# Performance work log

Measured on AMD Instinct MI355X. Metric: run time of the kernel, lower is better.

## Reference

```python
import jax, jax.numpy as jnp
from jax import lax
import numpy as np

# Config matching init_kwargs
NUM_CLASSES = 19
K = 200               # keep_k_centers
NMS_KERNEL = 9
CENTER_THR = 0.1
LABEL_DIV = 256
VOID = 255
STUFF_AREA = 4096
THING_IDS = np.array([11, 12, 13, 14, 15, 16, 17, 18])
IS_THING = jnp.zeros(NUM_CLASSES, bool).at[jnp.asarray(THING_IDS)].set(True)


def _process_one(logits, heat, offset):
    # logits [C,H,W], heat [1,H,W], offset [2,H,W]
    C, H, W = logits.shape
    sem = jnp.argmax(logits, axis=0).astype(jnp.int32)          # [H,W]
    h = heat[0]
    ht = jnp.where(h > CENTER_THR, h, 0.0)
    pad = NMS_KERNEL // 2
    # torch max_pool2d pads implicitly with -inf
    pooled = lax.reduce_window(ht, -jnp.inf, lax.max,
                               (NMS_KERNEL, NMS_KERNEL), (1, 1),
                               ((pad, pad), (pad, pad)))
    nms = jnp.where(ht == pooled, ht, 0.0)                      # [H,W]
    flat = nms.reshape(-1)
    scores, idx = lax.top_k(flat, K)                            # fixed-size center set
    valid = scores > 0.0
    num_pos = jnp.sum(flat > 0.0)
    # Match torch ordering: if more than K peaks -> topk (descending-score) order;
    # otherwise nonzero() row-major order. Invalid slots pushed to the end.
    big = jnp.int32(H * W + K)
    order_key = jnp.where(valid,
                          jnp.where(num_pos > K,
                                    jnp.arange(K, dtype=jnp.int32),
                                    idx.astype(jnp.int32)),
                          big)
    perm = jnp.argsort(order_key)
    idx = idx[perm]
    valid = valid[perm]
    FAR = 1e9  # invalid centers placed infinitely far away
    cy = jnp.where(valid, (idx // W).astype(jnp.float32), FAR)
    cx = jnp.where(valid, (idx % W).astype(jnp.float32), FAR)
    ty = jnp.arange(H, dtype=jnp.float32)[:, None] + offset[0]  # [H,W]
    tx = jnp.arange(W, dtype=jnp.float32)[None, :] + offset[1]  # [H,W]
    # squared distances [H,W,K]; argmin equals argmin of cdist
    d2 = (ty[..., None] - cy) ** 2 + (tx[..., None] - cx) ** 2
    closest = jnp.argmin(d2, axis=-1).astype(jnp.int32)         # [H,W]
    thing_mask = IS_THING[sem]
    inst = jnp.where(thing_mask & valid.any(), closest + 1, 0).astype(jnp.int32)
    # Majority class per instance via (instance, class) histogram.
    # argmax picks the smallest class among ties, matching torch.mode.
    hist = jnp.zeros((K + 1) * NUM_CLASSES, jnp.int32)
    hist = hist.at[(inst * NUM_CLASSES + sem).reshape(-1)].add(1)
    hist = hist.reshape(K + 1, NUM_CLASSES)
    majority = jnp.argmax(hist, axis=1).astype(jnp.int32)       # [K+1]
    pan = jnp.where(inst > 0, majority[inst] * LABEL_DIV + inst, VOID * LABEL_DIV)
    # Stuff: per-class pixel counts restricted to non-instance pixels
    stuff_pix = inst == 0
    skey = jnp.where(stuff_pix, sem, NUM_CLASSES).reshape(-1)
    scounts = jnp.zeros(NUM_CLASSES + 1, jnp.int32).at[skey].add(1)[:NUM_CLASSES]
    cond = stuff_pix & (~thing_mask) & (scounts[sem] >= STUFF_AREA)
    pan = jnp.where(cond, sem * LABEL_DIV, pan)
    return pan.astype(jnp.int32), inst


def setup_inputs() -> dict:
    key = jax.random.key(0)
    k1, k2, k3 = jax.random.split(key, 3)
    B, C, H, W = 2, NUM_CLASSES, 512, 1024
    semantic_logits = jax.random.normal(k1, (B, C, H, W), dtype=jnp.float32)
    center_heatmap = jax.random.uniform(k2, (B, 1, H, W), dtype=jnp.float32)
    offset_map = jax.random.normal(k3, (B, 2, H, W), dtype=jnp.float32)
    return {"semantic_logits": semantic_logits,
            "center_heatmap": center_heatmap,
            "offset_map": offset_map}


def reference(semantic_logits, center_heatmap, offset_map):
    pan, inst = jax.vmap(_process_one)(semantic_logits, center_heatmap, offset_map)
    return pan, inst
```

## Files before the change

### kernel.cpp

```cpp
#include <hip/hip_runtime.h>

#define B 2
#define C 19
#define H 512
#define W 1024
#define HW (H*W)
#define K 200
#define NCLS 19
#define HISTN ((K+1)*NCLS)
#define NT 512
#define MAXPB 128
#define SL 8192

typedef unsigned long long u64;


__global__ __launch_bounds__(256) void k_nms(const float* __restrict__ heat,
                                             u64* __restrict__ keys,
                                             int* __restrict__ pcnt) {
    __shared__ float ht[40][40];
    __shared__ float hm[40][32];
    __shared__ u64 lpk[1024];
    __shared__ int lcnt;
    int b = blockIdx.z;
    int x0 = blockIdx.x * 32, y0 = blockIdx.y * 32;
    int gb = b * NT + blockIdx.y * 32 + blockIdx.x;
    int tid = threadIdx.y * 32 + threadIdx.x;
    const float* hb = heat + (size_t)b * HW;
    if (tid == 0) lcnt = 0;
    for (int i = tid; i < 40 * 40; i += 256) {
        int ly = i / 40, lx = i % 40;
        int gy = y0 + ly - 4, gx = x0 + lx - 4;
        float v = 0.f;
        if (gy >= 0 && gy < H && gx >= 0 && gx < W) {
            float hv = hb[gy * W + gx];
            v = (hv > 0.1f) ? hv : 0.f;
        }
        ht[ly][lx] = v;
    }
    __syncthreads();
    for (int i = tid; i < 40 * 32; i += 256) {
        int ly = i >> 5, lx = i & 31;
        float m = ht[ly][lx];
#pragma unroll
        for (int d = 1; d < 9; ++d) m = fmaxf(m, ht[ly][lx + d]);
        hm[ly][lx] = m;
    }
    __syncthreads();
#pragma unroll
    for (int r = 0; r < 4; ++r) {
        int oy = threadIdx.y + r * 8;
        int ox = threadIdx.x;
        float c = ht[oy + 4][ox + 4];
        if (c > 0.f) {
            float m = hm[oy][ox];
#pragma unroll
            for (int d = 1; d < 9; ++d) m = fmaxf(m, hm[oy + d][ox]);
            if (c == m) {
                int pos = atomicAdd(&lcnt, 1);
                unsigned sb = __float_as_uint(c);
                lpk[pos] = ((u64)(~sb) << 19)
                         | (unsigned)((y0 + oy) * W + (x0 + ox));
            }
        }
    }
    __syncthreads();
    int n = (lcnt < MAXPB) ? lcnt : MAXPB;
    if (tid == 0) pcnt[gb] = n;
    for (int i = tid; i < n; i += 256)
        keys[(size_t)gb * MAXPB + i] = lpk[i];
}

__global__ __launch_bounds__(1024) void k_topk(const u64* __restrict__ keys,
                                               const int* __restrict__ pcnt,
                                               int* __restrict__ hist,
                                               int* __restrict__ anyv,
                                               float* __restrict__ cy,
                                               float* __restrict__ cx) {
    __shared__ u64 skeys[SL];
    __shared__ int hcnt[256];
    __shared__ u64 cand[256];
    __shared__ u64 s_thr;
    __shared__ int sR, gcnt, s_binc;
    __shared__ int wsum[8];
    int b = blockIdx.x, tid = threadIdx.x;
    int lane = tid & 63, w = tid >> 6;
    for (int i = tid; i < HISTN; i += 1024) hist[b * HISTN + i] = 0;
    int n = (tid < NT) ? pcnt[b * NT + tid] : 0;
    int incl = n;
#pragma unroll
    for (int off = 1; off < 64; off <<= 1) {
        int v = __shfl_up(incl, off, 64);
        if (lane >= off) incl += v;
    }
    if (tid < NT && lane == 63) wsum[w] = incl;
    __syncthreads();
    int N = 0;
#pragma unroll
    for (int j = 0; j < 8; ++j) N += wsum[j];
    int M = (N < SL) ? N : SL;
    if (tid < NT && n > 0) {
        int wbase = 0;
        for (int j = 0; j < w; ++j) wbase += wsum[j];
        int base = wbase + incl - n;
        const u64* src = keys + (size_t)(b * NT + tid) * MAXPB;
        for (int i = 0; i < n; ++i) {
            int d = base + i;
            if (d < SL) skeys[d] = src[i];
        }
    }
    if (tid == 0) { s_thr = 0ULL; sR = (M < K) ? M : K; gcnt = 0; }
    int Ksel = (M < K) ? M : K;
    __syncthreads();
    u64 thr;
    if (M <= K) {
        thr = ~0ULL;
    } else {
        bool done = false;
#pragma unroll 1
        for (int d = 48; d >= 0 && !done; d -= 8) {
            if (tid < 256) hcnt[tid] = 0;
            __syncthreads();
            u64 pref = s_thr;
            for (int i = tid; i < M; i += 1024) {
                u64 kk = skeys[i];
                int dig = (int)((kk >> d) & 255ULL);
                if (d == 48) {
                    u64 mask = __ballot(1);
                    while (mask) {
                        int leader = __ffsll(mask) - 1;
                        int d0 = __shfl(dig, leader, 64);
                        u64 same = __ballot(dig == d0);
                        if (lane == leader) atomicAdd(&hcnt[d0], (int)__popcll(same));
                        mask &= ~same;
                    }
                } else {
                    if ((kk >> (d + 8)) == (pref >> (d + 8)))
                        atomicAdd(&hcnt[dig], 1);
                }
            }
            __syncthreads();
            if (tid < 64) {
                int h0 = hcnt[tid * 4 + 0], h1 = hcnt[tid * 4 + 1];
                int h2 = hcnt[tid * 4 + 2], h3 = hcnt[tid * 4 + 3];
                int s = h0 + h1 + h2 + h3;
                int ic = s;
#pragma unroll
                for (int off = 1; off < 64; off <<= 1) {
                    int v = __shfl_up(ic, off, 64);
                    if (tid >= off) ic += v;
                }
                int R = sR;
                int before = ic - s;
                if (before < R && R <= ic) {
                    int c = before, t = tid * 4;
                    if (c + h0 < R) { c += h0; t++;
                        if (c + h1 < R) { c += h1; t++;
                            if (c + h2 < R) { c += h2; t++; } } }
                    s_thr = pref | ((u64)t << d);
                    sR = R - c;
                    s_binc = hcnt[t];
                }
            }
            __syncthreads();
            if (s_binc <= 256) {
                u64 p2 = s_thr;
                for (int i = tid; i < M; i += 1024) {
                    u64 kk = skeys[i];
                    if ((kk >> d) == (p2 >> d)) {
                        int p = atomicAdd(&gcnt, 1);
                        if (p < 256) cand[p] = kk;
                    }
                }
                __syncthreads();
                int g = (gcnt < 256) ? gcnt : 256;
                if (tid < g) {
                    u64 v = cand[tid];
                    int r = 0;
                    for (int j = 0; j < g; ++j) r += (int)(cand[j] < v);
                    if (r == sR - 1) s_thr = v;
                }
                __syncthreads();
                if (tid == 0) gcnt = 0;
                done = true;
                __syncthreads();
            }
        }
        thr = s_thr;
    }
    for (int i = tid; i < M; i += 1024) {
        u64 kk = skeys[i];
        if (kk <= thr) {
            int p = atomicAdd(&gcnt, 1);
            if (p < 256) cand[p] = kk;
        }
    }
    __syncthreads();
    if (tid < 256) {
        int g = (gcnt < 256) ? gcnt : 256;
        u64 v = (tid < g) ? cand[tid] : ~0ULL;
        if (N <= K && tid < g) v &= 0x7FFFFULL;
        cand[tid] = v;
    }
    __syncthreads();
    if (tid < 256) {
        u64 v = cand[tid];
        int r = 0;
        for (int j = 0; j < 256; ++j) {
            u64 cj = cand[j];
            r += (int)((cj < v) || (cj == v && j < tid));
        }
        skeys[r] = v;
    }
    __syncthreads();
    if (tid < K) {
        bool valid = tid < Ksel;
        unsigned idx = (unsigned)(skeys[tid] & 0x7FFFFULL);
        cy[b * K + tid] = valid ? (float)(idx >> 10) : 1e9f;
        cx[b * K + tid] = valid ? (float)(idx & 1023) : 1e9f;
    }
    if (tid == 0) anyv[b] = (N > 0) ? 1 : 0;
}

__global__ __launch_bounds__(128) void k_inst(const float* __restrict__ logits,
                                              const float* __restrict__ offs,
                                              const float* __restrict__ gcy,
                                              const float* __restrict__ gcx,
                                              const int* __restrict__ anyv,
                                              int* __restrict__ semout,
                                              int* __restrict__ inst,
                                              int* __restrict__ hist) {
    __shared__ int lh[HISTN];
    __shared__ float scy[K], scx[K];
    __shared__ unsigned char skk[K];
    __shared__ float red[2][8];
    __shared__ int wcnt[4];
    int b = blockIdx.z;
    int x0 = blockIdx.x << 5, y0 = blockIdx.y << 4;
    int tid = threadIdx.x;
    int lane = tid & 63, w = tid >> 6;
    for (int i = tid; i < HISTN; i += 128) lh[i] = 0;
    int r = tid >> 3;
    int c0 = (tid & 7) << 2;
    int gy = y0 + r;
    int gxb = x0 + c0;
    int q = (gy << 10) + gxb;
    const float* ob = offs + (size_t)b * 2 * HW;
    float4 oy4 = *(const float4*)(ob + q);
    float4 ox4 = *(const float4*)(ob + HW + q);
    int av = anyv[b];
    const float4* l4 = (const float4*)(logits + (size_t)b * C * HW) + (q >> 2);
    float4 v0 = l4[0];
    float best[4] = {v0.x, v0.y, v0.z, v0.w};
    int bc[4] = {0, 0, 0, 0};
#pragma unroll
    for (int c = 1; c < C; ++c) {
        float4 v = l4[(size_t)c * (HW / 4)];
        if (v.x > best[0]) { best[0] = v.x; bc[0] = c; }
        if (v.y > best[1]) { best[1] = v.y; bc[1] = c; }
        if (v.z > best[2]) { best[2] = v.z; bc[2] = c; }
        if (v.w > best[3]) { best[3] = v.w; bc[3] = c; }
    }
    float fy = (float)gy, fx = (float)gxb;
    float ty[4] = {fy + oy4.x, fy + oy4.y, fy + oy4.z, fy + oy4.w};
    float tx[4] = {fx + ox4.x, fx + 1.f + ox4.y, fx + 2.f + ox4.z, fx + 3.f + ox4.w};
    float tylo = fminf(fminf(ty[0], ty[1]), fminf(ty[2], ty[3]));
    float tyhi = fmaxf(fmaxf(ty[0], ty[1]), fmaxf(ty[2], ty[3]));
    float txlo = fminf(fminf(tx[0], tx[1]), fminf(tx[2], tx[3]));
    float txhi = fmaxf(fmaxf(tx[0], tx[1]), fmaxf(tx[2], tx[3]));
#pragma unroll
    for (int off = 32; off; off >>= 1) {
        tylo = fminf(tylo, __shfl_xor(tylo, off, 64));
        tyhi = fmaxf(tyhi, __shfl_xor(tyhi, off, 64));
        txlo = fminf(txlo, __shfl_xor(txlo, off, 64));
        txhi = fmaxf(txhi, __shfl_xor(txhi, off, 64));
    }
    if (lane == 0) { red[w][0] = tylo; red[w][1] = tyhi; red[w][2] = txlo; red[w][3] = txhi; }
    __syncthreads();
    tylo = fminf(red[0][0], red[1][0]);
    tyhi = fmaxf(red[0][1], red[1][1]);
    txlo = fminf(red[0][2], red[1][2]);
    txhi = fmaxf(red[0][3], red[1][3]);
    float kcy0 = gcy[b * K + tid], kcx0 = gcx[b * K + tid];
    float dmy = fmaxf(fmaxf(tylo - kcy0, kcy0 - tyhi), 0.f);
    float dMy = fmaxf(tyhi - kcy0, kcy0 - tylo);
    float dmx = fmaxf(fmaxf(txlo - kcx0, kcx0 - txhi), 0.f);
    float dMx = fmaxf(txhi - kcx0, kcx0 - txlo);
    float mind20 = dmy * dmy + dmx * dmx;
    float maxd20 = dMy * dMy + dMx * dMx;
    float kcy1 = 0.f, kcx1 = 0.f, mind21 = 0.f, maxd21 = 3.4e38f;
    if (tid < K - 128) {
        kcy1 = gcy[b * K + tid + 128]; kcx1 = gcx[b * K + tid + 128];
        float ay = fmaxf(fmaxf(tylo - kcy1, kcy1 - tyhi), 0.f);
        float My = fmaxf(tyhi - kcy1, kcy1 - tylo);
        float ax = fmaxf(fmaxf(txlo - kcx1, kcx1 - txhi), 0.f);
        float Mx = fmaxf(txhi - kcx1, kcx1 - txlo);
        mind21 = ay * ay + ax * ax;
        maxd21 = My * My + Mx * Mx;
    }
    float mv = fminf(maxd20, maxd21);
#pragma unroll
    for (int off = 32; off; off >>= 1) mv = fminf(mv, __shfl_xor(mv, off, 64));
    if (lane == 0) red[w][4] = mv;
    __syncthreads();
    float m = fminf(red[0][4], red[1][4]);
    float cut = m * 1.0001f + 1.0f;
    bool keep0 = mind20 <= cut;
    bool keep1 = (tid < K - 128) && (mind21 <= cut);
    u64 bal0 = __ballot(keep0);
    u64 bal1 = __ballot(keep1);
    if (lane == 0) { wcnt[w] = (int)__popcll(bal0); wcnt[2 + w] = (int)__popcll(bal1); }
    __syncthreads();
    int nk01 = wcnt[0] + wcnt[1];
    int nk = nk01 + wcnt[2] + wcnt[3];
    u64 low = (1ULL << lane) - 1ULL;
    if (keep0) {
        int rank = (w ? wcnt[0] : 0) + (int)__popcll(bal0 & low);
        scy[rank] = kcy0; scx[rank] = kcx0; skk[rank] = (unsigned char)tid;
    }
    if (keep1) {
        int rank = nk01 + (w ? wcnt[2] : 0) + (int)__popcll(bal1 & low);
        scy[rank] = kcy1; scx[rank] = kcx1; skk[rank] = (unsigned char)(tid + 128);
    }
    __syncthreads();
    float bd[4] = {3.4e38f, 3.4e38f, 3.4e38f, 3.4e38f};
    int bi[4] = {0, 0, 0, 0};
    if (av) {
        for (int i = 0; i < nk; ++i) {
            float cyk = scy[i], cxk = scx[i];
#pragma unroll
            for (int j = 0; j < 4; ++j) {
                float dy = __fsub_rn(ty[j], cyk);
                float dx = __fsub_rn(tx[j], cxk);
                float d2 = __fadd_rn(__fmul_rn(dy, dy), __fmul_rn(dx, dx));
                if (d2 < bd[j]) { bd[j] = d2; bi[j] = i; }
            }
        }
    }
    int4 sem4, inst4;
    int* semp = (int*)&sem4;
    int* instp = (int*)&inst4;
#pragma unroll
    for (int j = 0; j < 4; ++j) {
        int s = bc[j];
        int ins = (s >= 11 && av) ? ((int)skk[bi[j]] + 1) : 0;
        semp[j] = s;
        instp[j] = ins;
        atomicAdd(&lh[ins * NCLS + s], 1);
    }
    *(int4*)(semout + b * HW + q) = sem4;
    *(int4*)(inst + b * HW + q) = inst4;
    __syncthreads();
    for (int i = tid; i < HISTN; i += 128)
        if (lh[i]) atomicAdd(&hist[b * HISTN + i], lh[i]);
}

__global__ __launch_bounds__(256) void k_pan(int* __restrict__ pansem,
                                             const int* __restrict__ inst,
                                             const int* __restrict__ hist) {
    __shared__ int lh[HISTN];
    __shared__ unsigned char maj[K + 1];
    int b = blockIdx.x >> 8;
    int blk = blockIdx.x & 255;
    int tid = threadIdx.x;
    const int* hb = hist + b * HISTN;
    for (int i = tid; i < HISTN; i += 256) lh[i] = hb[i];
    __syncthreads();
    if (tid <= K) {
        const int* h = &lh[tid * NCLS];
        int best = h[0], bc = 0;
#pragma unroll
        for (int c = 1; c < NCLS; ++c)
            if (h[c] > best) { best = h[c]; bc = c; }
        maj[tid] = (unsigned char)bc;
    }
    __syncthreads();
    int p0 = b * HW + blk * 2048;
    const int4* s4 = (const int4*)(pansem + p0) + tid * 2;
    const int4* i4 = (const int4*)(inst + p0) + tid * 2;
    int4 sa = s4[0], sb = s4[1];
    int4 ia = i4[0], ib = i4[1];
    int4 pa, pb;
    int* sp = (int*)&sa; int* ip = (int*)&ia; int* pp = (int*)&pa;
#pragma unroll
    for (int j = 0; j < 4; ++j) {
        int s = sp[j], in_ = ip[j];
        int pan = (in_ > 0) ? ((int)maj[in_] * 256 + in_)
                 : ((s < 11 && lh[s] >= 4096) ? s * 256 : 65280);
        pp[j] = pan;
    }
    sp = (int*)&sb; ip = (int*)&ib; pp = (int*)&pb;
#pragma unroll
    for (int j = 0; j < 4; ++j) {
        int s = sp[j], in_ = ip[j];
        int pan = (in_ > 0) ? ((int)maj[in_] * 256 + in_)
                 : ((s < 11 && lh[s] >= 4096) ? s * 256 : 65280);
        pp[j] = pan;
    }
    ((int4*)(pansem + p0))[tid * 2] = pa;
    ((int4*)(pansem + p0))[tid * 2 + 1] = pb;
}

extern "C" void kernel_launch(void* const* d_in, const int* in_sizes, int n_in,
                              void* d_out, int out_size, void* d_ws, size_t ws_size,
                              hipStream_t stream) {
    const float* logits = (const float*)d_in[0];
    const float* heat   = (const float*)d_in[1];
    const float* offs   = (const float*)d_in[2];
    int* out = (int*)d_out;
    int* pansem = out;
    int* inst = out + B * HW;
    int* wsi = (int*)d_ws;
    int* hist = wsi;
    float* cy = (float*)(wsi + 8192);
    float* cx = cy + B * K;
    int* pcnt = wsi + 9216;
    int* anyv = wsi + 10496;
    u64* keys = (u64*)((char*)d_ws + 65536);

    k_nms<<<dim3(32, 16, B), dim3(32, 8, 1), 0, stream>>>(heat, keys, pcnt);
    k_topk<<<B, 1024, 0, stream>>>(keys, pcnt, hist, anyv, cy, cx);
    k_inst<<<dim3(32, 32, B), 128, 0, stream>>>(logits, offs, cy, cx, anyv, pansem, inst, hist);
    k_pan<<<B * 256, 256, 0, stream>>>(pansem, inst, hist);
}
```

Before: 79.60 us.

## Fuse NMS and top-k via last-block reduction; pack sem/inst into one buffer

Merges the NMS and top-k kernels into one launch. The last block to finish, found through an atomic counter, runs the top-k selection for both batches with 256 threads, and a union reuses the shared memory. k_inst now writes a single packed sem<<8|inst word per pixel instead of two arrays, and k_pan unpacks it and writes both outputs. This removes one kernel launch and one full-image write and read, at the cost of a serialized top-k on a single block with fewer threads, plus an extra memset launch for the counter.

```diff
diff --git a/kernel.cpp b/kernel.cpp
--- a/kernel.cpp
+++ b/kernel.cpp
@@ -10,22 +10,29 @@
 #define HISTN ((K+1)*NCLS)
 #define NT 512
 #define MAXPB 128
-#define SL 8192
+#define SL 6912
+#define NBLK (B*NT)
 
 typedef unsigned long long u64;
 
 
-__global__ __launch_bounds__(256) void k_nms(const float* __restrict__ heat,
-                                             u64* __restrict__ keys,
-                                             int* __restrict__ pcnt) {
-    __shared__ float ht[40][40];
-    __shared__ float hm[40][32];
-    __shared__ u64 lpk[1024];
-    __shared__ int lcnt;
+__global__ __launch_bounds__(256) void k_nms_topk(
+        const float* __restrict__ heat, u64* __restrict__ keys,
+        int* __restrict__ pcnt, int* __restrict__ done,
+        int* __restrict__ hist, int* __restrict__ anyv,
+        float* __restrict__ cy, float* __restrict__ cx) {
+    __shared__ union {
+        struct { float ht[40][40]; float hm[40][32]; u64 lpk[MAXPB]; } n;
+        struct { u64 skeys[SL]; u64 cand[256]; int hcnt[256]; int wsum[4]; } t;
+    } sh;
+    __shared__ int lcnt, amLast;
+    __shared__ u64 s_thr;
+    __shared__ int sR, gcnt, s_binc;
     int b = blockIdx.z;
     int x0 = blockIdx.x * 32, y0 = blockIdx.y * 32;
     int gb = b * NT + blockIdx.y * 32 + blockIdx.x;
     int tid = threadIdx.y * 32 + threadIdx.x;
+    int lane = tid & 63, w = tid >> 6;
     const float* hb = heat + (size_t)b * HW;
     if (tid == 0) lcnt = 0;
     for (int i = tid; i < 40 * 40; i += 256) {
@@ -36,31 +43,32 @@
             float hv = hb[gy * W + gx];
             v = (hv > 0.1f) ? hv : 0.f;
         }
-        ht[ly][lx] = v;
+        sh.n.ht[ly][lx] = v;
     }
     __syncthreads();
     for (int i = tid; i < 40 * 32; i += 256) {
         int ly = i >> 5, lx = i & 31;
-        float m = ht[ly][lx];
-#pragma unroll
-        for (int d = 1; d < 9; ++d) m = fmaxf(m, ht[ly][lx + d]);
-        hm[ly][lx] = m;
+        float m = sh.n.ht[ly][lx];
+#pragma unroll
+        for (int d = 1; d < 9; ++d) m = fmaxf(m, sh.n.ht[ly][lx + d]);
+        sh.n.hm[ly][lx] = m;
     }
     __syncthreads();
 #pragma unroll
     for (int r = 0; r < 4; ++r) {
         int oy = threadIdx.y + r * 8;
         int ox = threadIdx.x;
-        float c = ht[oy + 4][ox + 4];
+        float c = sh.n.ht[oy + 4][ox + 4];
         if (c > 0.f) {
-            float m = hm[oy][ox];
-#pragma unroll
-            for (int d = 1; d < 9; ++d) m = fmaxf(m, hm[oy + d][ox]);
+            float m = sh.n.hm[oy][ox];
+#pragma unroll
+            for (int d = 1; d < 9; ++d) m = fmaxf(m, sh.n.hm[oy + d][ox]);
             if (c == m) {
                 int pos = atomicAdd(&lcnt, 1);
                 unsigned sb = __float_as_uint(c);
-                lpk[pos] = ((u64)(~sb) << 19)
-                         | (unsigned)((y0 + oy) * W + (x0 + ox));
+                if (pos < MAXPB)
+                    sh.n.lpk[pos] = ((u64)(~sb) << 19)
+                                  | (unsigned)((y0 + oy) * W + (x0 + ox));
             }
         }
     }
@@ -68,158 +76,160 @@
     int n = (lcnt < MAXPB) ? lcnt : MAXPB;
     if (tid == 0) pcnt[gb] = n;
     for (int i = tid; i < n; i += 256)
-        keys[(size_t)gb * MAXPB + i] = lpk[i];
-}
-
-__global__ __launch_bounds__(1024) void k_topk(const u64* __restrict__ keys,
-                                               const int* __restrict__ pcnt,
-                                               int* __restrict__ hist,
-                                               int* __restrict__ anyv,
-                                               float* __restrict__ cy,
-                                               float* __restrict__ cx) {
-    __shared__ u64 skeys[SL];
-    __shared__ int hcnt[256];
-    __shared__ u64 cand[256];
-    __shared__ u64 s_thr;
-    __shared__ int sR, gcnt, s_binc;
-    __shared__ int wsum[8];
-    int b = blockIdx.x, tid = threadIdx.x;
-    int lane = tid & 63, w = tid >> 6;
-    for (int i = tid; i < HISTN; i += 1024) hist[b * HISTN + i] = 0;
-    int n = (tid < NT) ? pcnt[b * NT + tid] : 0;
-    int incl = n;
-#pragma unroll
-    for (int off = 1; off < 64; off <<= 1) {
-        int v = __shfl_up(incl, off, 64);
-        if (lane >= off) incl += v;
-    }
-    if (tid < NT && lane == 63) wsum[w] = incl;
-    __syncthreads();
-    int N = 0;
-#pragma unroll
-    for (int j = 0; j < 8; ++j) N += wsum[j];
-    int M = (N < SL) ? N : SL;
-    if (tid < NT && n > 0) {
+        keys[(size_t)gb * MAXPB + i] = sh.n.lpk[i];
+    __threadfence();
+    __syncthreads();
+    if (tid == 0) {
+        int old = atomicAdd(done, 1);
+        amLast = (old == NBLK - 1);
+    }
+    __syncthreads();
+    if (!amLast) return;
+    __threadfence();
+    __syncthreads();
+    for (int bb = 0; bb < B; ++bb) {
+        for (int i = tid; i < HISTN; i += 256) hist[bb * HISTN + i] = 0;
+        int t0 = 2 * tid;
+        int n0 = pcnt[bb * NT + t0], n1 = pcnt[bb * NT + t0 + 1];
+        int np = n0 + n1;
+        int incl = np;
+#pragma unroll
+        for (int off = 1; off < 64; off <<= 1) {
+            int v = __shfl_up(incl, off, 64);
+            if (lane >= off) incl += v;
+        }
+        if (lane == 63) sh.t.wsum[w] = incl;
+        __syncthreads();
+        int N = sh.t.wsum[0] + sh.t.wsum[1] + sh.t.wsum[2] + sh.t.wsum[3];
         int wbase = 0;
-        for (int j = 0; j < w; ++j) wbase += wsum[j];
-        int base = wbase + incl - n;
-        const u64* src = keys + (size_t)(b * NT + tid) * MAXPB;
-        for (int i = 0; i < n; ++i) {
+        for (int j = 0; j < w; ++j) wbase += sh.t.wsum[j];
+        int base = wbase + incl - np;
+        int M = (N < SL) ? N : SL;
+        const u64* src0 = keys + (size_t)(bb * NT + t0) * MAXPB;
+        for (int i = 0; i < n0; ++i) {
             int d = base + i;
-            if (d < SL) skeys[d] = src[i];
-        }
-    }
-    if (tid == 0) { s_thr = 0ULL; sR = (M < K) ? M : K; gcnt = 0; }
-    int Ksel = (M < K) ? M : K;
-    __syncthreads();
-    u64 thr;
-    if (M <= K) {
-        thr = ~0ULL;
-    } else {
-        bool done = false;
+            if (d < SL) sh.t.skeys[d] = src0[i];
+        }
+        const u64* src1 = keys + (size_t)(bb * NT + t0 + 1) * MAXPB;
+        for (int i = 0; i < n1; ++i) {
+            int d = base + n0 + i;
+            if (d < SL) sh.t.skeys[d] = src1[i];
+        }
+        if (tid == 0) { s_thr = 0ULL; sR = (M < K) ? M : K; gcnt = 0; }
+        int Ksel = (M < K) ? M : K;
+        __syncthreads();
+        u64 thr;
+        if (M <= K) {
+            thr = ~0ULL;
+        } else {
+            bool donep = false;
 #pragma unroll 1
-        for (int d = 48; d >= 0 && !done; d -= 8) {
-            if (tid < 256) hcnt[tid] = 0;
-            __syncthreads();
-            u64 pref = s_thr;
-            for (int i = tid; i < M; i += 1024) {
-                u64 kk = skeys[i];
-                int dig = (int)((kk >> d) & 255ULL);
-                if (d == 48) {
-                    u64 mask = __ballot(1);
-                    while (mask) {
-                        int leader = __ffsll(mask) - 1;
-                        int d0 = __shfl(dig, leader, 64);
-                        u64 same = __ballot(dig == d0);
-                        if (lane == leader) atomicAdd(&hcnt[d0], (int)__popcll(same));
-                        mask &= ~same;
-                    }
-                } else {
-                    if ((kk >> (d + 8)) == (pref >> (d + 8)))
-                        atomicAdd(&hcnt[dig], 1);
-                }
-            }
-            __syncthreads();
-            if (tid < 64) {
-                int h0 = hcnt[tid * 4 + 0], h1 = hcnt[tid * 4 + 1];
-                int h2 = hcnt[tid * 4 + 2], h3 = hcnt[tid * 4 + 3];
-                int s = h0 + h1 + h2 + h3;
-                int ic = s;
-#pragma unroll
-                for (int off = 1; off < 64; off <<= 1) {
-                    int v = __shfl_up(ic, off, 64);
-                    if (tid >= off) ic += v;
-                }
-                int R = sR;
-                int before = ic - s;
-                if (before < R && R <= ic) {
-                    int c = before, t = tid * 4;
-                    if (c + h0 < R) { c += h0; t++;
-                        if (c + h1 < R) { c += h1; t++;
-                            if (c + h2 < R) { c += h2; t++; } } }
-                    s_thr = pref | ((u64)t << d);
-                    sR = R - c;
-                    s_binc = hcnt[t];
-                }
-            }
-            __syncthreads();
-            if (s_binc <= 256) {
-                u64 p2 = s_thr;
-                for (int i = tid; i < M; i += 1024) {
-                    u64 kk = skeys[i];
-                    if ((kk >> d) == (p2 >> d)) {
-                        int p = atomicAdd(&gcnt, 1);
-                        if (p < 256) cand[p] = kk;
+            for (int d = 48; d >= 0 && !donep; d -= 8) {
+                sh.t.hcnt[tid] = 0;
+                __syncthreads();
+                u64 pref = s_thr;
+                for (int i = tid; i < M; i += 256) {
+                    u64 kk = sh.t.skeys[i];
+                    int dig = (int)((kk >> d) & 255ULL);
+                    if (d == 48) {
+                        u64 mask = __ballot(1);
+                        while (mask) {
+                            int leader = __ffsll(mask) - 1;
+                            int d0 = __shfl(dig, leader, 64);
+                            u64 same = __ballot(dig == d0);
+                            if (lane == leader)
+                                atomicAdd(&sh.t.hcnt[d0], (int)__popcll(same));
+                            mask &= ~same;
+                        }
+                    } else {
+                        if ((kk >> (d + 8)) == (pref >> (d + 8)))
+                            atomicAdd(&sh.t.hcnt[dig], 1);
                     }
                 }
                 __syncthreads();
-                int g = (gcnt < 256) ? gcnt : 256;
-                if (tid < g) {
-                    u64 v = cand[tid];
-                    int r = 0;
-                    for (int j = 0; j < g; ++j) r += (int)(cand[j] < v);
-                    if (r == sR - 1) s_thr = v;
+                if (tid < 64) {
+                    int h0 = sh.t.hcnt[tid * 4 + 0], h1 = sh.t.hcnt[tid * 4 + 1];
+                    int h2 = sh.t.hcnt[tid * 4 + 2], h3 = sh.t.hcnt[tid * 4 + 3];
+                    int s = h0 + h1 + h2 + h3;
+                    int ic = s;
+#pragma unroll
+                    for (int off = 1; off < 64; off <<= 1) {
+                        int v = __shfl_up(ic, off, 64);
+                        if (tid >= off) ic += v;
+                    }
+                    int R = sR;
+                    int before = ic - s;
+                    if (before < R && R <= ic) {
+                        int c = before, t = tid * 4;
+                        if (c + h0 < R) { c += h0; t++;
+                            if (c + h1 < R) { c += h1; t++;
+                                if (c + h2 < R) { c += h2; t++; } } }
+                        s_thr = pref | ((u64)t << d);
+                        sR = R - c;
+                        s_binc = sh.t.hcnt[t];
+                    }
                 }
                 __syncthreads();
-                if (tid == 0) gcnt = 0;
-                done = true;
-                __syncthreads();
+                if (s_binc <= 256) {
+                    u64 p2 = s_thr;
+                    for (int i = tid; i < M; i += 256) {
+                        u64 kk = sh.t.skeys[i];
+                        if ((kk >> d) == (p2 >> d)) {
+                            int p = atomicAdd(&gcnt, 1);
+                            if (p < 256) sh.t.cand[p] = kk;
+                        }
+                    }
+                    __syncthreads();
+                    int g = (gcnt < 256) ? gcnt : 256;
+                    if (tid < g) {
+                        u64 v = sh.t.cand[tid];
+                        int r = 0;
+                        for (int j = 0; j < g; ++j) r += (int)(sh.t.cand[j] < v);
+                        if (r == sR - 1) s_thr = v;
+                    }
+                    __syncthreads();
+                    if (tid == 0) gcnt = 0;
+                    donep = true;
+                    __syncthreads();
+                }
             }
-        }
-        thr = s_thr;
-    }
-    for (int i = tid; i < M; i += 1024) {
-        u64 kk = skeys[i];
-        if (kk <= thr) {
-            int p = atomicAdd(&gcnt, 1);
-            if (p < 256) cand[p] = kk;
-        }
-    }
-    __syncthreads();
-    if (tid < 256) {
-        int g = (gcnt < 256) ? gcnt : 256;
-        u64 v = (tid < g) ? cand[tid] : ~0ULL;
-        if (N <= K && tid < g) v &= 0x7FFFFULL;
-        cand[tid] = v;
-    }
-    __syncthreads();
-    if (tid < 256) {
-        u64 v = cand[tid];
-        int r = 0;
-        for (int j = 0; j < 256; ++j) {
-            u64 cj = cand[j];
-            r += (int)((cj < v) || (cj == v && j < tid));
-        }
-        skeys[r] = v;
-    }
-    __syncthreads();
-    if (tid < K) {
-        bool valid = tid < Ksel;
-        unsigned idx = (unsigned)(skeys[tid] & 0x7FFFFULL);
-        cy[b * K + tid] = valid ? (float)(idx >> 10) : 1e9f;
-        cx[b * K + tid] = valid ? (float)(idx & 1023) : 1e9f;
-    }
-    if (tid == 0) anyv[b] = (N > 0) ? 1 : 0;
+            thr = s_thr;
+        }
+        for (int i = tid; i < M; i += 256) {
+            u64 kk = sh.t.skeys[i];
+            if (kk <= thr) {
+                int p = atomicAdd(&gcnt, 1);
+                if (p < 256) sh.t.cand[p] = kk;
+            }
+        }
+        __syncthreads();
+        {
+            int g = (gcnt < 256) ? gcnt : 256;
+            u64 v = (tid < g) ? sh.t.cand[tid] : ~0ULL;
+            if (N <= K && tid < g) v &= 0x7FFFFULL;
+            __syncthreads();
+            sh.t.cand[tid] = v;
+        }
+        __syncthreads();
+        {
+            u64 v = sh.t.cand[tid];
+            int r = 0;
+            for (int j = 0; j < 256; ++j) {
+                u64 cj = sh.t.cand[j];
+                r += (int)((cj < v) || (cj == v && j < tid));
+            }
+            sh.t.skeys[r] = v;
+        }
+        __syncthreads();
+        if (tid < K) {
+            bool valid = tid < Ksel;
+            unsigned idx = (unsigned)(sh.t.skeys[tid] & 0x7FFFFULL);
+            cy[bb * K + tid] = valid ? (float)(idx >> 10) : 1e9f;
+            cx[bb * K + tid] = valid ? (float)(idx & 1023) : 1e9f;
+        }
+        if (tid == 0) anyv[bb] = (N > 0) ? 1 : 0;
+        __syncthreads();
+    }
 }
 
 __global__ __launch_bounds__(128) void k_inst(const float* __restrict__ logits,
@@ -227,8 +237,7 @@
                                               const float* __restrict__ gcy,
                                               const float* __restrict__ gcx,
                                               const int* __restrict__ anyv,
-                                              int* __restrict__ semout,
-                                              int* __restrict__ inst,
+                                              int* __restrict__ packed,
                                               int* __restrict__ hist) {
     __shared__ int lh[HISTN];
     __shared__ float scy[K], scx[K];
@@ -337,26 +346,23 @@
             }
         }
     }
-    int4 sem4, inst4;
-    int* semp = (int*)&sem4;
-    int* instp = (int*)&inst4;
+    int4 pk4;
+    int* pkp = (int*)&pk4;
 #pragma unroll
     for (int j = 0; j < 4; ++j) {
         int s = bc[j];
         int ins = (s >= 11 && av) ? ((int)skk[bi[j]] + 1) : 0;
-        semp[j] = s;
-        instp[j] = ins;
+        pkp[j] = (s << 8) | ins;
         atomicAdd(&lh[ins * NCLS + s], 1);
     }
-    *(int4*)(semout + b * HW + q) = sem4;
-    *(int4*)(inst + b * HW + q) = inst4;
+    *(int4*)(packed + b * HW + q) = pk4;
     __syncthreads();
     for (int i = tid; i < HISTN; i += 128)
         if (lh[i]) atomicAdd(&hist[b * HISTN + i], lh[i]);
 }
 
 __global__ __launch_bounds__(256) void k_pan(int* __restrict__ pansem,
-                                             const int* __restrict__ inst,
+                                             int* __restrict__ inst,
                                              const int* __restrict__ hist) {
     __shared__ int lh[HISTN];
     __shared__ unsigned char maj[K + 1];
@@ -376,29 +382,29 @@
     }
     __syncthreads();
     int p0 = b * HW + blk * 2048;
-    const int4* s4 = (const int4*)(pansem + p0) + tid * 2;
-    const int4* i4 = (const int4*)(inst + p0) + tid * 2;
-    int4 sa = s4[0], sb = s4[1];
-    int4 ia = i4[0], ib = i4[1];
-    int4 pa, pb;
-    int* sp = (int*)&sa; int* ip = (int*)&ia; int* pp = (int*)&pa;
+    const int4* s4 = (const int4*)(pansem + p0);
+    int4 pka = s4[tid * 2], pkb = s4[tid * 2 + 1];
+    int4 pa, pb, ia, ib;
+    int* kp = (int*)&pka; int* pp = (int*)&pa; int* ip = (int*)&ia;
 #pragma unroll
     for (int j = 0; j < 4; ++j) {
-        int s = sp[j], in_ = ip[j];
-        int pan = (in_ > 0) ? ((int)maj[in_] * 256 + in_)
-                 : ((s < 11 && lh[s] >= 4096) ? s * 256 : 65280);
-        pp[j] = pan;
-    }
-    sp = (int*)&sb; ip = (int*)&ib; pp = (int*)&pb;
+        int s = kp[j] >> 8, in_ = kp[j] & 255;
+        pp[j] = (in_ > 0) ? ((int)maj[in_] * 256 + in_)
+               : ((s < 11 && lh[s] >= 4096) ? s * 256 : 65280);
+        ip[j] = in_;
+    }
+    kp = (int*)&pkb; pp = (int*)&pb; ip = (int*)&ib;
 #pragma unroll
     for (int j = 0; j < 4; ++j) {
-        int s = sp[j], in_ = ip[j];
-        int pan = (in_ > 0) ? ((int)maj[in_] * 256 + in_)
-                 : ((s < 11 && lh[s] >= 4096) ? s * 256 : 65280);
-        pp[j] = pan;
+        int s = kp[j] >> 8, in_ = kp[j] & 255;
+        pp[j] = (in_ > 0) ? ((int)maj[in_] * 256 + in_)
+               : ((s < 11 && lh[s] >= 4096) ? s * 256 : 65280);
+        ip[j] = in_;
     }
     ((int4*)(pansem + p0))[tid * 2] = pa;
     ((int4*)(pansem + p0))[tid * 2 + 1] = pb;
+    ((int4*)(inst + p0))[tid * 2] = ia;
+    ((int4*)(inst + p0))[tid * 2 + 1] = ib;
 }
 
 extern "C" void kernel_launch(void* const* d_in, const int* in_sizes, int n_in,
@@ -411,15 +417,17 @@
     int* pansem = out;
     int* inst = out + B * HW;
     int* wsi = (int*)d_ws;
-    int* hist = wsi;
+    int* done = wsi;
+    int* hist = wsi + 16;
     float* cy = (float*)(wsi + 8192);
     float* cx = cy + B * K;
     int* pcnt = wsi + 9216;
     int* anyv = wsi + 10496;
     u64* keys = (u64*)((char*)d_ws + 65536);
 
-    k_nms<<<dim3(32, 16, B), dim3(32, 8, 1), 0, stream>>>(heat, keys, pcnt);
-    k_topk<<<B, 1024, 0, stream>>>(keys, pcnt, hist, anyv, cy, cx);
-    k_inst<<<dim3(32, 32, B), 128, 0, stream>>>(logits, offs, cy, cx, anyv, pansem, inst, hist);
+    hipMemsetAsync(done, 0, 16, stream);
+    k_nms_topk<<<dim3(32, 16, B), dim3(32, 8, 1), 0, stream>>>(
+        heat, keys, pcnt, done, hist, anyv, cy, cx);
+    k_inst<<<dim3(32, 32, B), 128, 0, stream>>>(logits, offs, cy, cx, anyv, pansem, hist);
     k_pan<<<B * 256, 256, 0, stream>>>(pansem, inst, hist);
 }
```

Measured after the change: 198.6 us. +149.5%, slower.

## Compact NMS peaks via global atomic and pack sem/inst into one intermediate

Applied to the files above, without the earlier changes.

NMS blocks now append their peaks to a compact per-batch key list through a global atomic counter, replacing fixed per-block slots. The top-k kernel then loads the list directly instead of running a prefix-scan gather. Semantic class and instance id are packed into one int in k_inst, so only one full-size intermediate array is written and read, and k_pan writes the instance output itself. This adds a memset launch and makes key order nondeterministic, which is harmless because keys are selected by value. Keys past the shared-memory limit are read from global memory.

```diff
diff --git a/kernel.cpp b/kernel.cpp
--- a/kernel.cpp
+++ b/kernel.cpp
@@ -6,25 +6,24 @@
 #define W 1024
 #define HW (H*W)
 #define K 200
+#define CAPK 8192
+#define SL 6912
 #define NCLS 19
 #define HISTN ((K+1)*NCLS)
-#define NT 512
-#define MAXPB 128
-#define SL 8192
+#define MAXPB 256
 
 typedef unsigned long long u64;
 
 
 __global__ __launch_bounds__(256) void k_nms(const float* __restrict__ heat,
                                              u64* __restrict__ keys,
-                                             int* __restrict__ pcnt) {
+                                             int* __restrict__ cnt) {
     __shared__ float ht[40][40];
     __shared__ float hm[40][32];
-    __shared__ u64 lpk[1024];
-    __shared__ int lcnt;
+    __shared__ u64 lpk[MAXPB];
+    __shared__ int lcnt, gbase;
     int b = blockIdx.z;
     int x0 = blockIdx.x * 32, y0 = blockIdx.y * 32;
-    int gb = b * NT + blockIdx.y * 32 + blockIdx.x;
     int tid = threadIdx.y * 32 + threadIdx.x;
     const float* hb = heat + (size_t)b * HW;
     if (tid == 0) lcnt = 0;
@@ -59,20 +58,24 @@
             if (c == m) {
                 int pos = atomicAdd(&lcnt, 1);
                 unsigned sb = __float_as_uint(c);
-                lpk[pos] = ((u64)(~sb) << 19)
-                         | (unsigned)((y0 + oy) * W + (x0 + ox));
+                if (pos < MAXPB)
+                    lpk[pos] = ((u64)(~sb) << 19)
+                             | (unsigned)((y0 + oy) * W + (x0 + ox));
             }
         }
     }
     __syncthreads();
     int n = (lcnt < MAXPB) ? lcnt : MAXPB;
-    if (tid == 0) pcnt[gb] = n;
-    for (int i = tid; i < n; i += 256)
-        keys[(size_t)gb * MAXPB + i] = lpk[i];
+    if (tid == 0 && n > 0) gbase = atomicAdd(&cnt[b], n);
+    __syncthreads();
+    for (int i = tid; i < n; i += 256) {
+        int gp = gbase + i;
+        if (gp < CAPK) keys[(size_t)b * CAPK + gp] = lpk[i];
+    }
 }
 
 __global__ __launch_bounds__(1024) void k_topk(const u64* __restrict__ keys,
-                                               const int* __restrict__ pcnt,
+                                               const int* __restrict__ cnt,
                                                int* __restrict__ hist,
                                                int* __restrict__ anyv,
                                                float* __restrict__ cy,
@@ -82,48 +85,28 @@
     __shared__ u64 cand[256];
     __shared__ u64 s_thr;
     __shared__ int sR, gcnt, s_binc;
-    __shared__ int wsum[8];
     int b = blockIdx.x, tid = threadIdx.x;
-    int lane = tid & 63, w = tid >> 6;
+    int lane = tid & 63;
     for (int i = tid; i < HISTN; i += 1024) hist[b * HISTN + i] = 0;
-    int n = (tid < NT) ? pcnt[b * NT + tid] : 0;
-    int incl = n;
-#pragma unroll
-    for (int off = 1; off < 64; off <<= 1) {
-        int v = __shfl_up(incl, off, 64);
-        if (lane >= off) incl += v;
-    }
-    if (tid < NT && lane == 63) wsum[w] = incl;
-    __syncthreads();
-    int N = 0;
-#pragma unroll
-    for (int j = 0; j < 8; ++j) N += wsum[j];
-    int M = (N < SL) ? N : SL;
-    if (tid < NT && n > 0) {
-        int wbase = 0;
-        for (int j = 0; j < w; ++j) wbase += wsum[j];
-        int base = wbase + incl - n;
-        const u64* src = keys + (size_t)(b * NT + tid) * MAXPB;
-        for (int i = 0; i < n; ++i) {
-            int d = base + i;
-            if (d < SL) skeys[d] = src[i];
-        }
-    }
-    if (tid == 0) { s_thr = 0ULL; sR = (M < K) ? M : K; gcnt = 0; }
+    const u64* kb = keys + (size_t)b * CAPK;
+    int N = cnt[b];
+    int M = (N < CAPK) ? N : CAPK;
     int Ksel = (M < K) ? M : K;
+    for (int i = tid; i < M && i < SL; i += 1024) skeys[i] = kb[i];
+    if (tid == 0) { s_thr = 0ULL; sR = Ksel; gcnt = 0; }
     __syncthreads();
     u64 thr;
     if (M <= K) {
         thr = ~0ULL;
     } else {
-        bool done = false;
+        bool donep = false;
 #pragma unroll 1
-        for (int d = 48; d >= 0 && !done; d -= 8) {
+        for (int d = 48; d >= 0 && !donep; d -= 8) {
             if (tid < 256) hcnt[tid] = 0;
             __syncthreads();
             u64 pref = s_thr;
             for (int i = tid; i < M; i += 1024) {
-                u64 kk = skeys[i];
+                u64 kk = (i < SL) ? skeys[i] : kb[i];
                 int dig = (int)((kk >> d) & 255ULL);
                 if (d == 48) {
                     u64 mask = __ballot(1);
@@ -166,7 +149,7 @@
             if (s_binc <= 256) {
                 u64 p2 = s_thr;
                 for (int i = tid; i < M; i += 1024) {
-                    u64 kk = skeys[i];
+                    u64 kk = (i < SL) ? skeys[i] : kb[i];
                     if ((kk >> d) == (p2 >> d)) {
                         int p = atomicAdd(&gcnt, 1);
                         if (p < 256) cand[p] = kk;
@@ -182,14 +165,14 @@
                 }
                 __syncthreads();
                 if (tid == 0) gcnt = 0;
-                done = true;
+                donep = true;
                 __syncthreads();
             }
         }
         thr = s_thr;
     }
     for (int i = tid; i < M; i += 1024) {
-        u64 kk = skeys[i];
+        u64 kk = (i < SL) ? skeys[i] : kb[i];
         if (kk <= thr) {
             int p = atomicAdd(&gcnt, 1);
             if (p < 256) cand[p] = kk;
@@ -206,6 +189,7 @@
     if (tid < 256) {
         u64 v = cand[tid];
         int r = 0;
+#pragma unroll 8
         for (int j = 0; j < 256; ++j) {
             u64 cj = cand[j];
             r += (int)((cj < v) || (cj == v && j < tid));
@@ -227,8 +211,7 @@
                                               const float* __restrict__ gcy,
                                               const float* __restrict__ gcx,
                                               const int* __restrict__ anyv,
-                                              int* __restrict__ semout,
-                                              int* __restrict__ inst,
+                                              int* __restrict__ packed,
                                               int* __restrict__ hist) {
     __shared__ int lh[HISTN];
     __shared__ float scy[K], scx[K];
@@ -337,26 +320,23 @@
             }
         }
     }
-    int4 sem4, inst4;
-    int* semp = (int*)&sem4;
-    int* instp = (int*)&inst4;
+    int4 pk4;
+    int* pkp = (int*)&pk4;
 #pragma unroll
     for (int j = 0; j < 4; ++j) {
         int s = bc[j];
         int ins = (s >= 11 && av) ? ((int)skk[bi[j]] + 1) : 0;
-        semp[j] = s;
-        instp[j] = ins;
+        pkp[j] = (s << 8) | ins;
         atomicAdd(&lh[ins * NCLS + s], 1);
     }
-    *(int4*)(semout + b * HW + q) = sem4;
-    *(int4*)(inst + b * HW + q) = inst4;
+    *(int4*)(packed + b * HW + q) = pk4;
     __syncthreads();
     for (int i = tid; i < HISTN; i += 128)
         if (lh[i]) atomicAdd(&hist[b * HISTN + i], lh[i]);
 }
 
 __global__ __launch_bounds__(256) void k_pan(int* __restrict__ pansem,
-                                             const int* __restrict__ inst,
+                                             int* __restrict__ inst,
                                              const int* __restrict__ hist) {
     __shared__ int lh[HISTN];
     __shared__ unsigned char maj[K + 1];
@@ -376,29 +356,29 @@
     }
     __syncthreads();
     int p0 = b * HW + blk * 2048;
-    const int4* s4 = (const int4*)(pansem + p0) + tid * 2;
-    const int4* i4 = (const int4*)(inst + p0) + tid * 2;
-    int4 sa = s4[0], sb = s4[1];
-    int4 ia = i4[0], ib = i4[1];
-    int4 pa, pb;
-    int* sp = (int*)&sa; int* ip = (int*)&ia; int* pp = (int*)&pa;
+    const int4* s4 = (const int4*)(pansem + p0);
+    int4 pka = s4[tid * 2], pkb = s4[tid * 2 + 1];
+    int4 pa, pb, ia, ib;
+    int* kp = (int*)&pka; int* pp = (int*)&pa; int* ip = (int*)&ia;
 #pragma unroll
     for (int j = 0; j < 4; ++j) {
-        int s = sp[j], in_ = ip[j];
-        int pan = (in_ > 0) ? ((int)maj[in_] * 256 + in_)
-                 : ((s < 11 && lh[s] >= 4096) ? s * 256 : 65280);
-        pp[j] = pan;
-    }
-    sp = (int*)&sb; ip = (int*)&ib; pp = (int*)&pb;
+        int s = kp[j] >> 8, in_ = kp[j] & 255;
+        pp[j] = (in_ > 0) ? ((int)maj[in_] * 256 + in_)
+               : ((s < 11 && lh[s] >= 4096) ? s * 256 : 65280);
+        ip[j] = in_;
+    }
+    kp = (int*)&pkb; pp = (int*)&pb; ip = (int*)&ib;
 #pragma unroll
     for (int j = 0; j < 4; ++j) {
-        int s = sp[j], in_ = ip[j];
-        int pan = (in_ > 0) ? ((int)maj[in_] * 256 + in_)
-                 : ((s < 11 && lh[s] >= 4096) ? s * 256 : 65280);
-        pp[j] = pan;
+        int s = kp[j] >> 8, in_ = kp[j] & 255;
+        pp[j] = (in_ > 0) ? ((int)maj[in_] * 256 + in_)
+               : ((s < 11 && lh[s] >= 4096) ? s * 256 : 65280);
+        ip[j] = in_;
     }
     ((int4*)(pansem + p0))[tid * 2] = pa;
     ((int4*)(pansem + p0))[tid * 2 + 1] = pb;
+    ((int4*)(inst + p0))[tid * 2] = ia;
+    ((int4*)(inst + p0))[tid * 2 + 1] = ib;
 }
 
 extern "C" void kernel_launch(void* const* d_in, const int* in_sizes, int n_in,
@@ -411,15 +391,16 @@
     int* pansem = out;
     int* inst = out + B * HW;
     int* wsi = (int*)d_ws;
-    int* hist = wsi;
+    int* cnt  = wsi;
+    int* hist = wsi + 16;
     float* cy = (float*)(wsi + 8192);
     float* cx = cy + B * K;
-    int* pcnt = wsi + 9216;
     int* anyv = wsi + 10496;
     u64* keys = (u64*)((char*)d_ws + 65536);
 
-    k_nms<<<dim3(32, 16, B), dim3(32, 8, 1), 0, stream>>>(heat, keys, pcnt);
-    k_topk<<<B, 1024, 0, stream>>>(keys, pcnt, hist, anyv, cy, cx);
-    k_inst<<<dim3(32, 32, B), 128, 0, stream>>>(logits, offs, cy, cx, anyv, pansem, inst, hist);
+    hipMemsetAsync(cnt, 0, 16, stream);
+    k_nms<<<dim3(32, 16, B), dim3(32, 8, 1), 0, stream>>>(heat, keys, cnt);
+    k_topk<<<B, 1024, 0, stream>>>(keys, cnt, hist, anyv, cy, cx);
+    k_inst<<<dim3(32, 32, B), 128, 0, stream>>>(logits, offs, cy, cx, anyv, pansem, hist);
     k_pan<<<B * 256, 256, 0, stream>>>(pansem, inst, hist);
 }
```

Measured after the change: 91.47 us. 1.15x slower.
